# Optimization experiments

Hardware: AMD Instinct MI355X
Metric: run time of the kernel (lower is better)

## Reference

```python
import jax, jax.numpy as jnp
import numpy as np

D_MODEL = 1024
N_HEADS = 16
HEAD_DIM = D_MODEL // N_HEADS
EPS = 1e-6


def setup_inputs() -> dict:
    key = jax.random.key(0)
    k1, k2, k3 = jax.random.split(key, 3)
    b, l, d = 2, 2048, D_MODEL
    x = jax.random.normal(k1, (b, l, d), dtype=jnp.float32)
    # Linear weights stored so that y = x @ W (no bias), matching torch math
    w_qkv = jax.random.normal(k2, (d, 3 * d), dtype=jnp.float32) * (1.0 / np.sqrt(d))
    w_proj = jax.random.normal(k3, (d, d), dtype=jnp.float32) * (1.0 / np.sqrt(d))
    norm_w = jnp.ones((d,), dtype=jnp.float32)
    return {"x": x, "norm_w": norm_w, "w_qkv": w_qkv, "w_proj": w_proj}


def rms_norm(x, w, eps=EPS):
    x32 = x.astype(jnp.float32)
    inv_rms = jax.lax.rsqrt(jnp.mean(x32 * x32, axis=-1, keepdims=True) + eps)
    return (x32 * inv_rms).astype(x.dtype) * w.astype(x.dtype)


def reference(x, norm_w, w_qkv, w_proj):
    b, l, d = x.shape
    h = rms_norm(x, norm_w)
    qkv = h @ w_qkv                       # [b, l, 3d]
    q, k, v = jnp.split(qkv, 3, axis=-1)

    def heads(t):
        return t.reshape(b, l, N_HEADS, HEAD_DIM).transpose(0, 2, 1, 3)  # [b,h,l,hd]

    q, k, v = heads(q), heads(k), heads(v)
    scale = 1.0 / np.sqrt(HEAD_DIM)
    scores = jnp.einsum('bhqd,bhkd->bhqk', q, k) * scale  # full LxL scores
    attn = jax.nn.softmax(scores, axis=-1)
    ctx = jnp.einsum('bhqk,bhkd->bhqd', attn, v)
    ctx = ctx.transpose(0, 2, 1, 3).reshape(b, l, d)
    out = ctx @ w_proj
    return x + out
```

## Files before the change

### kernel.cpp

```cpp
#include <hip/hip_runtime.h>
#include <hip/hip_bf16.h>
#include <cstdint>
#include <cstddef>

typedef __attribute__((ext_vector_type(8))) short bf16x8;
typedef __attribute__((ext_vector_type(4))) float f32x4;
typedef __attribute__((ext_vector_type(16))) float f32x16;
typedef __attribute__((ext_vector_type(2))) float fv2;

#define GLD_LDS16(gptr, lptr)                                                  \
  __builtin_amdgcn_global_load_lds(                                            \
      (const __attribute__((address_space(1))) void*)(gptr),                   \
      (__attribute__((address_space(3))) void*)(lptr), 16, 0, 0)

__device__ __forceinline__ uint32_t cvtpk(float a, float b) {
  uint32_t d;
  asm("v_cvt_pk_bf16_f32 %0, %1, %2" : "=v"(d) : "v"(a), "v"(b));
  return d;
}

__device__ __forceinline__ fv2 pkadd(fv2 a, fv2 b) {
  fv2 d;
  asm("v_pk_add_f32 %0, %1, %2" : "=v"(d) : "v"(a), "v"(b));
  return d;
}

__device__ __forceinline__ float xhalf_max(float x) {
  auto r = __builtin_amdgcn_permlane32_swap(__float_as_uint(x),
                                            __float_as_uint(x), false, false);
  return fmaxf(__uint_as_float(r[0]), __uint_as_float(r[1]));
}

__device__ __forceinline__ float xhalf_sum(float x) {
  auto r = __builtin_amdgcn_permlane32_swap(__float_as_uint(x),
                                            __float_as_uint(x), false, false);
  return __uint_as_float(r[0]) + __uint_as_float(r[1]);
}

__global__ __launch_bounds__(256) void rmsnorm_kernel(
    const float* __restrict__ x, const float* __restrict__ w,
    __hip_bfloat16* __restrict__ h) {
  const int row = blockIdx.x;
  const int tid = threadIdx.x;
  const float4 v = reinterpret_cast<const float4*>(x + (size_t)row * 1024)[tid];
  float ss = v.x * v.x + v.y * v.y + v.z * v.z + v.w * v.w;
#pragma unroll
  for (int off = 32; off >= 1; off >>= 1) ss += __shfl_down(ss, off);
  __shared__ float red[4];
  if ((tid & 63) == 0) red[tid >> 6] = ss;
  __syncthreads();
  const float inv =
      rsqrtf((red[0] + red[1] + red[2] + red[3]) * (1.0f / 1024.0f) + 1e-6f);
  const float4 wv = reinterpret_cast<const float4*>(w)[tid];
  __hip_bfloat16* hp = h + (size_t)row * 1024 + tid * 4;
  hp[0] = __float2bfloat16(v.x * inv * wv.x);
  hp[1] = __float2bfloat16(v.y * inv * wv.y);
  hp[2] = __float2bfloat16(v.z * inv * wv.z);
  hp[3] = __float2bfloat16(v.w * inv * wv.w);
}

__global__ __launch_bounds__(256) void transpose_cast2_kernel(
    const float* __restrict__ w_qkv, const float* __restrict__ w_proj,
    __hip_bfloat16* __restrict__ wqkvT, __hip_bfloat16* __restrict__ wprojT) {
  __shared__ float tile[32][33];
  const float* src;
  __hip_bfloat16* dst;
  int C, bx;
  if (blockIdx.x < 96) {
    src = w_qkv; dst = wqkvT; C = 3072; bx = blockIdx.x * 32;
  } else {
    src = w_proj; dst = wprojT; C = 1024; bx = (blockIdx.x - 96) * 32;
  }
  const int R = 1024;
  const int by = blockIdx.y * 32;
  const int tx = threadIdx.x;
  const int ty = threadIdx.y;
#pragma unroll
  for (int j = 0; j < 32; j += 8)
    tile[ty + j][tx] = src[(size_t)(by + ty + j) * C + bx + tx];
  __syncthreads();
#pragma unroll
  for (int j = 0; j < 32; j += 8)
    dst[(size_t)(bx + ty + j) * R + by + tx] = __float2bfloat16(tile[tx][ty + j]);
}

template <int BM, int BN, int RESID>
__device__ __forceinline__ void gemm_tile(
    const __hip_bfloat16* __restrict__ A, const __hip_bfloat16* __restrict__ BT,
    void* __restrict__ Cout, const float* __restrict__ resid, int M, int N,
    int K, int bx, int by, __hip_bfloat16* As, __hip_bfloat16* Bs) {
  const int tid = threadIdx.x;
  const int lane = tid & 63;
  const int wid = tid >> 6;
  const int m0 = by * BM;
  const int n0 = bx * BN;
  const int wr = wid >> 1, wc = wid & 1;
  constexpr int MI = BM / 32, NJ = BN / 32;
  constexpr int NCHA = BM / 16, NCHB = BN / 16;
  f32x4 acc[MI][NJ] = {};
  const int nk = K >> 5;
  const int lr = lane & 15, lk = lane >> 4;
  for (int kt = 0; kt < nk; ++kt) {
#pragma unroll
    for (int it = 0; it < NCHA / 4; ++it) {
      const int c = wid + it * 4;
      const int e = c * 512 + lane * 8;
      GLD_LDS16(A + (size_t)(m0 + (e >> 5)) * K + kt * 32 + (e & 31),
                As + c * 512);
    }
#pragma unroll
    for (int it = 0; it < NCHB / 4; ++it) {
      const int c = wid + it * 4;
      const int e = c * 512 + lane * 8;
      GLD_LDS16(BT + (size_t)(n0 + (e >> 5)) * K + kt * 32 + (e & 31),
                Bs + c * 512);
    }
    __syncthreads();
    bf16x8 af[MI], bfr[NJ];
#pragma unroll
    for (int i = 0; i < MI; ++i)
      af[i] = *(const bf16x8*)(As + (wr * (BM / 2) + i * 16 + lr) * 32 + lk * 8);
#pragma unroll
    for (int j = 0; j < NJ; ++j)
      bfr[j] = *(const bf16x8*)(Bs + (wc * (BN / 2) + j * 16 + lr) * 32 + lk * 8);
#pragma unroll
    for (int i = 0; i < MI; ++i)
#pragma unroll
      for (int j = 0; j < NJ; ++j)
        acc[i][j] = __builtin_amdgcn_mfma_f32_16x16x32_bf16(af[i], bfr[j],
                                                            acc[i][j], 0, 0, 0);
    __syncthreads();
  }
#pragma unroll
  for (int i = 0; i < MI; ++i)
#pragma unroll
    for (int j = 0; j < NJ; ++j)
#pragma unroll
      for (int r = 0; r < 4; ++r) {
        const int row = m0 + wr * (BM / 2) + i * 16 + lk * 4 + r;
        const int col = n0 + wc * (BN / 2) + j * 16 + lr;
        const float v = acc[i][j][r];
        if (RESID) {
          ((float*)Cout)[(size_t)row * N + col] =
              resid[(size_t)row * N + col] + v;
        } else {
          ((__hip_bfloat16*)Cout)[(size_t)row * N + col] = __float2bfloat16(v);
        }
      }
}

__global__ __launch_bounds__(256) void qkv_gemm_kernel(
    const __hip_bfloat16* __restrict__ h, const __hip_bfloat16* __restrict__ wqkT,
    const __hip_bfloat16* __restrict__ wvT, __hip_bfloat16* __restrict__ qkbuf,
    __hip_bfloat16* __restrict__ vTbuf) {
  __shared__ __align__(16) __hip_bfloat16 As[128 * 32];
  __shared__ __align__(16) __hip_bfloat16 Bs[128 * 32];
  const int bid = blockIdx.x;
  if (bid < 512) {
    const int xcd = bid & 7, seq = bid >> 3;
    const int by = xcd * 4 + (seq >> 4);
    const int bx = seq & 15;
    gemm_tile<128, 128, 0>(h, wqkT, (void*)qkbuf, nullptr, 4096, 2048, 1024,
                           bx, by, As, Bs);
  } else {
    const int t = bid - 512;
    const int xcd = t & 7, seq = t >> 3;
    const int by = xcd * 2 + (seq >> 5);
    const int bx = seq & 31;
    gemm_tile<64, 128, 0>(wvT, h, (void*)vTbuf, nullptr, 1024, 4096, 1024, bx,
                          by, As, Bs);
  }
}

__global__ __launch_bounds__(256) void proj_gemm_kernel(
    const __hip_bfloat16* __restrict__ ctx, const __hip_bfloat16* __restrict__ wpT,
    float* __restrict__ out, const float* __restrict__ x) {
  __shared__ __align__(16) __hip_bfloat16 As[128 * 32];
  __shared__ __align__(16) __hip_bfloat16 Bs[64 * 32];
  const int bid = blockIdx.x;
  const int xcd = bid & 7, seq = bid >> 3;
  const int by = xcd * 4 + (seq >> 4);
  const int bx = seq & 15;
  gemm_tile<128, 64, 1>(ctx, wpT, (void*)out, x, 4096, 1024, 1024, bx, by, As,
                        Bs);
}

__global__ __launch_bounds__(256, 2) void attn_kernel(
    const __hip_bfloat16* __restrict__ qk, const __hip_bfloat16* __restrict__ vT,
    __hip_bfloat16* __restrict__ ctx) {
  const int flat = blockIdx.x;
  const int xcd = flat & 7, seq = flat >> 3;
  const int bh = xcd * 4 + (seq >> 4);
  const int qt = seq & 15;
  const int b = bh >> 4, h = bh & 15;
  const int tid = threadIdx.x, lane = tid & 63, wid = tid >> 6;
  const size_t tok0 = (size_t)b * 2048;
  const int q0 = qt * 128 + wid * 32;
  const int l31 = lane & 31;
  const int hi = lane >> 5;

  __shared__ __align__(16) char Kl[2][64 * 128];
  __shared__ __align__(16) char Vl[2][64 * 128];

  const int sr = tid >> 2;
  const int scB = (tid & 3) * 32;
  const int swW = (sr & 7) << 4;
  const int wA = sr * 128 + (scB ^ swW);
  const int wB = sr * 128 + ((scB + 16) ^ swW);

  const __hip_bfloat16* kbase = qk + tok0 * 2048 + 1024 + (size_t)h * 64;
  const __hip_bfloat16* vbase = vT + ((size_t)(h * 64 + sr)) * 4096 + tok0;
  const int scE = (tid & 3) * 16;

  bf16x8 qf[4];
  {
    const __hip_bfloat16* qptr = qk + (tok0 + q0 + l31) * 2048 + h * 64 + hi * 8;
    const float c = 0.125f * 1.44269504f;
#pragma unroll
    for (int ks = 0; ks < 4; ++ks) {
      bf16x8 v = *(const bf16x8*)(qptr + ks * 16);
      const __hip_bfloat16* ie = (const __hip_bfloat16*)&v;
      __hip_bfloat16* oe = (__hip_bfloat16*)&qf[ks];
#pragma unroll
      for (int i = 0; i < 8; ++i)
        oe[i] = __float2bfloat16(__bfloat162float(ie[i]) * c);
    }
  }

  const int swR = (l31 & 7) << 4;
  const int rb0 = l31 * 128;
  const int rb1 = (32 + l31) * 128;

  bf16x8 kreg0, kreg1, vreg0, vreg1;
  auto load_tile = [&](int t) {
    const __hip_bfloat16* kp = kbase + (size_t)(t * 64 + sr) * 2048 + scE;
    kreg0 = *(const bf16x8*)kp;
    kreg1 = *(const bf16x8*)(kp + 8);
    const __hip_bfloat16* vp = vbase + t * 64 + scE;
    vreg0 = *(const bf16x8*)vp;
    vreg1 = *(const bf16x8*)(vp + 8);
  };
  auto write_tile = [&](int bf) {
    *(bf16x8*)(Kl[bf] + wA) = kreg0;
    *(bf16x8*)(Kl[bf] + wB) = kreg1;
    *(bf16x8*)(Vl[bf] + wA) = vreg0;
    *(bf16x8*)(Vl[bf] + wB) = vreg1;
  };

  f32x16 oT0 = {}, oT1 = {};
  float mrow = -3e38f, lrow = 0.f;

  load_tile(0);
  write_tile(0);
  __syncthreads();

  for (int kvt = 0; kvt < 32; ++kvt) {
    const int cur = kvt & 1;
    if (kvt + 1 < 32) load_tile(kvt + 1);

    f32x16 s0 = {}, s1 = {};
#pragma unroll
    for (int ks = 0; ks < 4; ++ks) {
      const int cOff = (ks * 32 + hi * 16) ^ swR;
      const bf16x8 kf0 = *(const bf16x8*)(Kl[cur] + rb0 + cOff);
      const bf16x8 kf1 = *(const bf16x8*)(Kl[cur] + rb1 + cOff);
      s0 = __builtin_amdgcn_mfma_f32_32x32x16_bf16(kf0, qf[ks], s0, 0, 0, 0);
      s1 = __builtin_amdgcn_mfma_f32_32x32x16_bf16(kf1, qf[ks], s1, 0, 0, 0);
    }

    const float m0_ = fmaxf(fmaxf(s0[0], s0[1]), s0[2]);
    const float m1_ = fmaxf(fmaxf(s0[3], s0[4]), s0[5]);
    const float m2_ = fmaxf(fmaxf(s0[6], s0[7]), s0[8]);
    const float m3_ = fmaxf(fmaxf(s0[9], s0[10]), s0[11]);
    const float m4_ = fmaxf(fmaxf(s0[12], s0[13]), s0[14]);
    const float m5_ = fmaxf(fmaxf(s0[15], s1[0]), s1[1]);
    const float m6_ = fmaxf(fmaxf(s1[2], s1[3]), s1[4]);
    const float m7_ = fmaxf(fmaxf(s1[5], s1[6]), s1[7]);
    const float m8_ = fmaxf(fmaxf(s1[8], s1[9]), s1[10]);
    const float m9_ = fmaxf(fmaxf(s1[11], s1[12]), s1[13]);
    const float ma_ = fmaxf(s1[14], s1[15]);
    const float n0_ = fmaxf(fmaxf(m0_, m1_), m2_);
    const float n1_ = fmaxf(fmaxf(m3_, m4_), m5_);
    const float n2_ = fmaxf(fmaxf(m6_, m7_), m8_);
    const float n3_ = fmaxf(m9_, ma_);
    float mx = fmaxf(fmaxf(fmaxf(n0_, n1_), n2_), n3_);
    mx = xhalf_max(mx);

    const bool grow = (mx - mrow) > 8.0f;
    if (__any(grow)) {
      const float mn = fmaxf(mrow, mx);
      const float alpha = __builtin_amdgcn_exp2f(mrow - mn);
      mrow = mn;
      lrow *= alpha;
#pragma unroll
      for (int i = 0; i < 16; ++i) {
        oT0[i] *= alpha;
        oT1[i] *= alpha;
      }
    }

    const fv2 nm2 = {-mrow, -mrow};
    union {
      f32x16 v;
      fv2 p[8];
    } U0, U1;
    U0.v = s0;
    U1.v = s1;
#pragma unroll
    for (int i = 0; i < 8; ++i) {
      U0.p[i] = pkadd(U0.p[i], nm2);
      U1.p[i] = pkadd(U1.p[i], nm2);
    }
    float ps = 0.f;
    uint32_t pk0[8], pk1[8];
#pragma unroll
    for (int i = 0; i < 8; ++i) {
      const float a0 = __builtin_amdgcn_exp2f(U0.p[i].x);
      const float a1 = __builtin_amdgcn_exp2f(U0.p[i].y);
      const float b0 = __builtin_amdgcn_exp2f(U1.p[i].x);
      const float b1 = __builtin_amdgcn_exp2f(U1.p[i].y);
      ps += (a0 + a1) + (b0 + b1);
      pk0[i] = cvtpk(a0, a1);
      pk1[i] = cvtpk(b0, b1);
    }
    lrow += xhalf_sum(ps);

#pragma unroll
    for (int ts = 0; ts < 4; ++ts) {
      const uint32_t* pk = (ts < 2) ? pk0 : pk1;
      const int o = (ts & 1) * 4;
      auto w02 = __builtin_amdgcn_permlane32_swap(pk[o], pk[o + 2], false, false);
      auto w13 =
          __builtin_amdgcn_permlane32_swap(pk[o + 1], pk[o + 3], false, false);
      uint32_t fr[4] = {w02[0], w13[0], w02[1], w13[1]};
      const bf16x8 pf = *(const bf16x8*)fr;
      const int cOff = (ts * 32 + hi * 16) ^ swR;
      const bf16x8 vf0 = *(const bf16x8*)(Vl[cur] + rb0 + cOff);
      const bf16x8 vf1 = *(const bf16x8*)(Vl[cur] + rb1 + cOff);
      oT0 = __builtin_amdgcn_mfma_f32_32x32x16_bf16(vf0, pf, oT0, 0, 0, 0);
      oT1 = __builtin_amdgcn_mfma_f32_32x32x16_bf16(vf1, pf, oT1, 0, 0, 0);
    }

    if (kvt + 1 < 32) write_tile(cur ^ 1);
    __syncthreads();
  }

  const float linv = 1.0f / lrow;
  __hip_bfloat16* cb = ctx + (tok0 + q0 + l31) * 1024 + h * 64;
#pragma unroll
  for (int dh = 0; dh < 2; ++dh) {
#pragma unroll
    for (int rq = 0; rq < 4; ++rq) {
      const int d0 = 8 * rq + 4 * hi + 32 * dh;
      float v0, v1, v2, v3;
      if (dh) {
        v0 = oT1[4 * rq];
        v1 = oT1[4 * rq + 1];
        v2 = oT1[4 * rq + 2];
        v3 = oT1[4 * rq + 3];
      } else {
        v0 = oT0[4 * rq];
        v1 = oT0[4 * rq + 1];
        v2 = oT0[4 * rq + 2];
        v3 = oT0[4 * rq + 3];
      }
      *(uint32_t*)(cb + d0) = cvtpk(v0 * linv, v1 * linv);
      *(uint32_t*)(cb + d0 + 2) = cvtpk(v2 * linv, v3 * linv);
    }
  }
}

extern "C" void kernel_launch(void* const* d_in, const int* in_sizes, int n_in,
                              void* d_out, int out_size, void* d_ws,
                              size_t ws_size, hipStream_t stream) {
  const float* x = (const float*)d_in[0];
  const float* norm_w = (const float*)d_in[1];
  const float* w_qkv = (const float*)d_in[2];
  const float* w_proj = (const float*)d_in[3];
  float* out = (float*)d_out;

  char* ws = (char*)d_ws;
  __hip_bfloat16* hbuf = (__hip_bfloat16*)(ws);
  __hip_bfloat16* wqkvT = (__hip_bfloat16*)(ws + (size_t)8 * 1024 * 1024);
  __hip_bfloat16* wprojT = (__hip_bfloat16*)(ws + (size_t)14 * 1024 * 1024);
  __hip_bfloat16* qkbuf = (__hip_bfloat16*)(ws + (size_t)16 * 1024 * 1024);
  __hip_bfloat16* vTbuf = (__hip_bfloat16*)(ws + (size_t)32 * 1024 * 1024);
  __hip_bfloat16* ctx = (__hip_bfloat16*)(ws + (size_t)40 * 1024 * 1024);

  rmsnorm_kernel<<<dim3(4096), dim3(256), 0, stream>>>(x, norm_w, hbuf);
  transpose_cast2_kernel<<<dim3(128, 32), dim3(32, 8), 0, stream>>>(
      w_qkv, w_proj, wqkvT, wprojT);
  qkv_gemm_kernel<<<dim3(1024), dim3(256), 0, stream>>>(
      hbuf, wqkvT, wqkvT + (size_t)2048 * 1024, qkbuf, vTbuf);
  attn_kernel<<<dim3(512), dim3(256), 0, stream>>>(qkbuf, vTbuf, ctx);
  proj_gemm_kernel<<<dim3(512), dim3(256), 0, stream>>>(ctx, wprojT, out, x);
}
```

Measured before the change: 128.6 us.

## Split attention KV range in two halves and merge with combine kernel

Each attention block now processes only half of the key/value sequence, doubling the grid from 512 to 1024 blocks. Each block writes partial normalized outputs plus per-row max and sum statistics, and a new combine kernel merges the two halves with log-sum-exp weights. The aim is better occupancy and load balance on the many CUs of the device. In exchange it adds an extra kernel launch, extra global traffic for the partial outputs, and reuses workspace buffers (hbuf and the qkv weight area) as scratch.

```diff
diff --git a/kernel.cpp b/kernel.cpp
--- a/kernel.cpp
+++ b/kernel.cpp
@@ -35,6 +35,10 @@
   auto r = __builtin_amdgcn_permlane32_swap(__float_as_uint(x),
                                             __float_as_uint(x), false, false);
   return __uint_as_float(r[0]) + __uint_as_float(r[1]);
+}
+
+__device__ __forceinline__ float b2f(short s) {
+  return __uint_as_float(((uint32_t)(uint16_t)s) << 16);
 }
 
 __global__ __launch_bounds__(256) void rmsnorm_kernel(
@@ -187,14 +191,18 @@
 
 __global__ __launch_bounds__(256, 2) void attn_kernel(
     const __hip_bfloat16* __restrict__ qk, const __hip_bfloat16* __restrict__ vT,
-    __hip_bfloat16* __restrict__ ctx) {
+    __hip_bfloat16* __restrict__ po0, __hip_bfloat16* __restrict__ po1,
+    float2* __restrict__ mlbuf) {
   const int flat = blockIdx.x;
   const int xcd = flat & 7, seq = flat >> 3;
-  const int bh = xcd * 4 + (seq >> 4);
-  const int qt = seq & 15;
+  const int bh = xcd * 4 + (seq >> 5);
+  const int r2 = seq & 31;
+  const int half = r2 & 1;
+  const int qt = r2 >> 1;
   const int b = bh >> 4, h = bh & 15;
   const int tid = threadIdx.x, lane = tid & 63, wid = tid >> 6;
   const size_t tok0 = (size_t)b * 2048;
+  const size_t tokH = tok0 + half * 1024;
   const int q0 = qt * 128 + wid * 32;
   const int l31 = lane & 31;
   const int hi = lane >> 5;
@@ -208,8 +216,8 @@
   const int wA = sr * 128 + (scB ^ swW);
   const int wB = sr * 128 + ((scB + 16) ^ swW);
 
-  const __hip_bfloat16* kbase = qk + tok0 * 2048 + 1024 + (size_t)h * 64;
-  const __hip_bfloat16* vbase = vT + ((size_t)(h * 64 + sr)) * 4096 + tok0;
+  const __hip_bfloat16* kbase = qk + tokH * 2048 + 1024 + (size_t)h * 64;
+  const __hip_bfloat16* vbase = vT + ((size_t)(h * 64 + sr)) * 4096 + tokH;
   const int scE = (tid & 3) * 16;
 
   bf16x8 qf[4];
@@ -254,9 +262,9 @@
   write_tile(0);
   __syncthreads();
 
-  for (int kvt = 0; kvt < 32; ++kvt) {
+  for (int kvt = 0; kvt < 16; ++kvt) {
     const int cur = kvt & 1;
-    if (kvt + 1 < 32) load_tile(kvt + 1);
+    if (kvt + 1 < 16) load_tile(kvt + 1);
 
     f32x16 s0 = {}, s1 = {};
 #pragma unroll
@@ -341,12 +349,13 @@
       oT1 = __builtin_amdgcn_mfma_f32_32x32x16_bf16(vf1, pf, oT1, 0, 0, 0);
     }
 
-    if (kvt + 1 < 32) write_tile(cur ^ 1);
+    if (kvt + 1 < 16) write_tile(cur ^ 1);
     __syncthreads();
   }
 
   const float linv = 1.0f / lrow;
-  __hip_bfloat16* cb = ctx + (tok0 + q0 + l31) * 1024 + h * 64;
+  const size_t tok = tok0 + q0 + l31;
+  __hip_bfloat16* pb = (half ? po1 : po0) + tok * 1024 + h * 64;
 #pragma unroll
   for (int dh = 0; dh < 2; ++dh) {
 #pragma unroll
@@ -364,10 +373,42 @@
         v2 = oT0[4 * rq + 2];
         v3 = oT0[4 * rq + 3];
       }
-      *(uint32_t*)(cb + d0) = cvtpk(v0 * linv, v1 * linv);
-      *(uint32_t*)(cb + d0 + 2) = cvtpk(v2 * linv, v3 * linv);
-    }
-  }
+      *(uint32_t*)(pb + d0) = cvtpk(v0 * linv, v1 * linv);
+      *(uint32_t*)(pb + d0 + 2) = cvtpk(v2 * linv, v3 * linv);
+    }
+  }
+  if (hi == 0) {
+    float2 v;
+    v.x = mrow;
+    v.y = lrow;
+    mlbuf[tok * 32 + h * 2 + half] = v;
+  }
+}
+
+__global__ __launch_bounds__(256) void combine_kernel(
+    const __hip_bfloat16* __restrict__ po0, __hip_bfloat16* __restrict__ ctx,
+    const float2* __restrict__ mlbuf) {
+  const size_t e = ((size_t)blockIdx.x * 256 + threadIdx.x) * 8;
+  const int row = (int)(e >> 10), col = (int)(e & 1023);
+  const int h2 = (col >> 6) * 2;
+  const float2 ml0 = mlbuf[(size_t)row * 32 + h2];
+  const float2 ml1 = mlbuf[(size_t)row * 32 + h2 + 1];
+  const float mc = fmaxf(ml0.x, ml1.x);
+  float w0 = __builtin_amdgcn_exp2f(ml0.x - mc) * ml0.y;
+  float w1 = __builtin_amdgcn_exp2f(ml1.x - mc) * ml1.y;
+  const float inv = 1.0f / (w0 + w1);
+  w0 *= inv;
+  w1 *= inv;
+  const bf16x8 a = *(const bf16x8*)(po0 + e);
+  const bf16x8 c = *(const bf16x8*)(ctx + e);
+  uint32_t r[4];
+#pragma unroll
+  for (int i = 0; i < 4; ++i) {
+    const float x0 = b2f(a[2 * i]) * w0 + b2f(c[2 * i]) * w1;
+    const float x1 = b2f(a[2 * i + 1]) * w0 + b2f(c[2 * i + 1]) * w1;
+    r[i] = cvtpk(x0, x1);
+  }
+  *(bf16x8*)(ctx + e) = *(const bf16x8*)r;
 }
 
 extern "C" void kernel_launch(void* const* d_in, const int* in_sizes, int n_in,
@@ -386,12 +427,17 @@
   __hip_bfloat16* qkbuf = (__hip_bfloat16*)(ws + (size_t)16 * 1024 * 1024);
   __hip_bfloat16* vTbuf = (__hip_bfloat16*)(ws + (size_t)32 * 1024 * 1024);
   __hip_bfloat16* ctx = (__hip_bfloat16*)(ws + (size_t)40 * 1024 * 1024);
+  __hip_bfloat16* po0 = hbuf;
+  __hip_bfloat16* po1 = ctx;
+  float2* mlbuf = (float2*)wqkvT;
 
   rmsnorm_kernel<<<dim3(4096), dim3(256), 0, stream>>>(x, norm_w, hbuf);
   transpose_cast2_kernel<<<dim3(128, 32), dim3(32, 8), 0, stream>>>(
       w_qkv, w_proj, wqkvT, wprojT);
   qkv_gemm_kernel<<<dim3(1024), dim3(256), 0, stream>>>(
       hbuf, wqkvT, wqkvT + (size_t)2048 * 1024, qkbuf, vTbuf);
-  attn_kernel<<<dim3(512), dim3(256), 0, stream>>>(qkbuf, vTbuf, ctx);
+  attn_kernel<<<dim3(1024), dim3(256), 0, stream>>>(qkbuf, vTbuf, po0, po1,
+                                                    mlbuf);
+  combine_kernel<<<dim3(2048), dim3(256), 0, stream>>>(po0, po1, mlbuf);
   proj_gemm_kernel<<<dim3(512), dim3(256), 0, stream>>>(ctx, wprojT, out, x);
 }
```

Result: slower. 134.6 us (+4.7%).
